# Performance work log

Measured on AMD Instinct MI355X. Metric: run time of the kernel, lower is better.

The kernel has to match this reference:

```python
import jax, jax.numpy as jnp
import numpy as np

ANGSTROM_TO_BOHR = 1.8897261258369282
CUTOFF = 5.2  # angstrom
N_SPECIES = 4  # H, C, N, O

# GFN1-xTB-style per-element constants for (H, C, N, O)
_ALPHA = np.array([2.209700, 1.247655, 1.524329, 1.845886], dtype=np.float32)
_Y_EFF = np.array([1.116244, 4.428763, 5.498808, 5.171786], dtype=np.float32)


def _smooth_cutoff(d, rc, eps=1e-10):
    # torchani 'smooth' cutoff: exp(1 - 1/(1 - (d/rc)^2)) for d < rc, else 0
    x2 = (d / rc) ** 2
    e = 1.0 - 1.0 / jnp.maximum(1.0 - x2, eps)
    return jnp.where(d < rc, jnp.exp(e), jnp.zeros_like(d))


def setup_inputs() -> dict:
    key = jax.random.key(0)
    k1, k2, k3 = jax.random.split(key, 3)
    M, A, P = 2048, 64, 8388608
    element_idxs = jax.random.randint(k1, (M, A), 0, N_SPECIES, dtype=jnp.int64)
    neighbor_idxs = jax.random.randint(k2, (2, P), 0, M * A, dtype=jnp.int64)
    distances = jax.random.uniform(k3, (P,), dtype=jnp.float32, minval=0.5, maxval=6.0)
    # precomputed pairwise parameter tables (buffers in the torch module)
    y_ab = jnp.asarray(np.outer(_Y_EFF, _Y_EFF))                 # [4,4]
    sqrt_alpha_ab = jnp.asarray(np.sqrt(np.outer(_ALPHA, _ALPHA)))  # [4,4]
    k_rep = np.full((N_SPECIES, N_SPECIES), 1.5, dtype=np.float32)
    k_rep[0, 0] = 1.0  # H-H
    k_rep_ab = jnp.asarray(k_rep)
    return {
        "element_idxs": element_idxs,
        "neighbor_idxs": neighbor_idxs,
        "distances": distances,
        "y_ab": y_ab,
        "sqrt_alpha_ab": sqrt_alpha_ab,
        "k_rep_ab": k_rep_ab,
    }


def reference(element_idxs, neighbor_idxs, distances, y_ab, sqrt_alpha_ab, k_rep_ab):
    M, A = element_idxs.shape
    d = jnp.clip(distances, 1e-7) * ANGSTROM_TO_BOHR  # [P] bohr
    species12 = element_idxs.reshape(-1)[neighbor_idxs]  # [2, P]
    s0, s1 = species12[0], species12[1]
    y = y_ab[s0, s1]                    # [P] gather
    sa = sqrt_alpha_ab[s0, s1]          # [P]
    kr = k_rep_ab[s0, s1]               # [P]
    rep = (y / d) * jnp.exp(-sa * d ** kr)
    rep = rep * _smooth_cutoff(d, CUTOFF * ANGSTROM_TO_BOHR)
    mol_idx = neighbor_idxs[0] // A     # [P]
    energies = jax.ops.segment_sum(rep, mol_idx, num_segments=M)  # [M]
    return energies
```

## Files before the change

kernel.cpp:

```cpp
#include <hip/hip_runtime.h>


#define AB_D 1.8897261258369282
#define L2E  1.4426950408889634f

__global__ __launch_bounds__(256) void pack_zero_kernel(
    const int* __restrict__ elem, int natoms, int nwords,
    unsigned* __restrict__ packed, float* __restrict__ out, int M)
{
    int g = blockIdx.x * blockDim.x + threadIdx.x;
    if (g < M) out[g] = 0.0f;
    if (packed != nullptr && g < nwords) {
        int base = g * 16;
        unsigned w = 0u;
        if (base + 16 <= natoms) {
            const int4* p = (const int4*)(elem + base);
            #pragma unroll
            for (int q = 0; q < 4; ++q) {
                int4 v = p[q];
                w |= ((unsigned)v.x & 3u) << (2 * (4 * q + 0));
                w |= ((unsigned)v.y & 3u) << (2 * (4 * q + 1));
                w |= ((unsigned)v.z & 3u) << (2 * (4 * q + 2));
                w |= ((unsigned)v.w & 3u) << (2 * (4 * q + 3));
            }
        } else {
            for (int j = 0; j < 16; ++j) {
                int a = base + j;
                unsigned s = (a < natoms) ? ((unsigned)elem[a] & 3u) : 0u;
                w |= s << (2 * j);
            }
        }
        packed[g] = w;
    }
}

__global__ __launch_bounds__(1024, 8) void rep_main_kernel(
    const int* __restrict__ nbr, const float* __restrict__ dist,
    const unsigned* __restrict__ packed_g,
    const float* __restrict__ y_ab, const float* __restrict__ sa_ab,
    const float* __restrict__ kr_ab,
    long long P, int M, int nwords, int ashift, int A,
    float* __restrict__ partials, float* __restrict__ out,
    int mode )
{
    extern __shared__ char smem[];
    float*  acc = (float*)smem;
    float2* tbl = (float2*)(smem + (size_t)M * 4);
    unsigned* pk = (unsigned*)(smem + (size_t)M * 4 + 16 * sizeof(float2));

    const int tid = threadIdx.x;
    const int nthr = blockDim.x;

    for (int m = tid; m < M; m += nthr) acc[m] = 0.0f;
    for (int w = tid; w < nwords; w += nthr) pk[w] = packed_g[w];
    if (tid < 16) {
        float sa = sa_ab[tid] * L2E;
        if (kr_ab[tid] == 1.0f) sa = -sa;
        tbl[tid] = make_float2(y_ab[tid], sa);
    }
    __syncthreads();

    const float ABf    = (float)AB_D;
    const float DMIN   = (float)(1e-7 * AB_D);
    const float RC     = (float)(5.2 * AB_D);
    const float RCINV  = (float)(1.0 / (5.2 * AB_D));
    const int* nb0 = nbr;
    const int* nb1 = nbr + P;

    auto process = [&](int a0, int a1, float draw) {
        float d = fmaxf(draw * ABf, DMIN);
        if (d < RC) {
            unsigned ua0 = (unsigned)a0, ua1 = (unsigned)a1;
            unsigned w0 = pk[ua0 >> 4];
            unsigned w1 = pk[ua1 >> 4];
            unsigned s0 = (w0 >> ((ua0 & 15u) * 2u)) & 3u;
            unsigned s1 = (w1 >> ((ua1 & 15u) * 2u)) & 3u;
            float2 t = tbl[s0 * 4u + s1];

            float sq   = __builtin_amdgcn_sqrtf(d);
            float fac  = (t.y < 0.0f) ? 1.0f : sq;
            float drep = d * fac;
            float x    = d * RCINV;
            float om   = fmaf(-x, x, 1.0f);
            float r    = __builtin_amdgcn_rcpf(om);
            float e    = fmaf(-L2E, r, L2E);
            float arg  = fmaf(-fabsf(t.y), drep, e);
            float ex   = __builtin_amdgcn_exp2f(arg);
            float rep  = t.x * __builtin_amdgcn_rcpf(d) * ex;

            unsigned mol = (ashift >= 0) ? (ua0 >> ashift) : (ua0 / (unsigned)A);
            atomicAdd(&acc[mol], rep);
        }
    };

    long long P4 = P >> 2;
    long long gstride = (long long)gridDim.x * nthr;
    for (long long q = (long long)blockIdx.x * nthr + tid; q < P4; q += gstride) {
        int4   i0 = ((const int4*)nb0)[q];
        int4   i1 = ((const int4*)nb1)[q];
        float4 dv = ((const float4*)dist)[q];
        process(i0.x, i1.x, dv.x);
        process(i0.y, i1.y, dv.y);
        process(i0.z, i1.z, dv.z);
        process(i0.w, i1.w, dv.w);
    }
    long long tail0 = P4 << 2;
    if (blockIdx.x == 0) {
        for (long long p = tail0 + tid; p < P; p += nthr)
            process(nb0[p], nb1[p], dist[p]);
    }
    __syncthreads();

    if (mode == 0) {
        float* row = partials + (size_t)blockIdx.x * (size_t)M;
        for (int m = tid; m < M; m += nthr) row[m] = acc[m];
    } else {
        for (int m = tid; m < M; m += nthr) {
            float v = acc[m];
            if (v != 0.0f) atomicAdd(&out[m], v);
        }
    }
}

__global__ __launch_bounds__(256) void reduce_kernel(
    const float* __restrict__ partials, float* __restrict__ out,
    int M, int nblk, int rows_per)
{
    int m = blockIdx.x * blockDim.x + threadIdx.x;
    if (m >= M) return;
    int r0 = blockIdx.y * rows_per;
    int r1 = r0 + rows_per;
    if (r1 > nblk) r1 = nblk;
    if (r0 >= r1) return;
    float s0 = 0.f, s1 = 0.f, s2 = 0.f, s3 = 0.f;
    int r = r0;
    for (; r + 3 < r1; r += 4) {
        s0 += partials[(size_t)(r + 0) * M + m];
        s1 += partials[(size_t)(r + 1) * M + m];
        s2 += partials[(size_t)(r + 2) * M + m];
        s3 += partials[(size_t)(r + 3) * M + m];
    }
    for (; r < r1; ++r) s0 += partials[(size_t)r * M + m];
    atomicAdd(&out[m], (s0 + s1) + (s2 + s3));
}

extern "C" void kernel_launch(void* const* d_in, const int* in_sizes, int n_in,
                              void* d_out, int out_size, void* d_ws, size_t ws_size,
                              hipStream_t stream)
{
    const int*   elem  = (const int*)d_in[0];
    const int*   nbr   = (const int*)d_in[1];
    const float* dist  = (const float*)d_in[2];
    const float* y_ab  = (const float*)d_in[3];
    const float* sa_ab = (const float*)d_in[4];
    const float* kr_ab = (const float*)d_in[5];
    float* out = (float*)d_out;

    const int natoms = in_sizes[0];
    const long long P = (long long)in_sizes[2];
    const int M = out_size;
    const int A = natoms / M;
    int ashift = -1;
    if (A > 0 && (A & (A - 1)) == 0) {
        int s = 0;
        while ((1 << s) < A) ++s;
        ashift = s;
    }
    const int nwords = (natoms + 15) / 16;

    size_t packed_bytes = ((size_t)nwords * 4 + 255) & ~(size_t)255;
    bool have_packed = (ws_size >= packed_bytes);
    unsigned* packed = have_packed ? (unsigned*)d_ws : nullptr;
    if (!have_packed) return;

    const int BLOCK = 1024;
    int nblk = 512;
    float* partials = nullptr;
    int mode = 1;
    {
        size_t avail = ws_size - packed_bytes;
        size_t rowb = (size_t)M * 4;
        long long maxrows = (long long)(avail / rowb);
        if (maxrows >= 64) {
            nblk = (int)(maxrows < 512 ? maxrows : 512);
            partials = (float*)((char*)d_ws + packed_bytes);
            mode = 0;
        }
    }

    {
        int total = (nwords > M) ? nwords : M;
        int g = (total + 255) / 256;
        hipLaunchKernelGGL(pack_zero_kernel, dim3(g), dim3(256), 0, stream,
                           elem, natoms, nwords, packed, out, M);
    }

    {
        size_t smem = (size_t)M * 4 + 16 * sizeof(float2) + (size_t)nwords * 4;
        hipLaunchKernelGGL(rep_main_kernel, dim3(nblk), dim3(BLOCK), smem, stream,
                           nbr, dist, packed, y_ab, sa_ab, kr_ab,
                           P, M, nwords, ashift, A, partials, out, mode);
    }

    if (mode == 0) {
        const int SPLIT = 32;
        int rows_per = (nblk + SPLIT - 1) / SPLIT;
        dim3 grid((M + 255) / 256, SPLIT);
        hipLaunchKernelGGL(reduce_kernel, grid, dim3(256), 0, stream,
                           partials, out, M, nblk, rows_per);
    }
}
```

Baseline: 154.7 us.

## Software-pipeline pair loads and make the per-pair cutoff math branchless

The grid-stride loop now prefetches the next iteration's index and distance vectors before processing the current ones, with a sched_barrier to keep the loads issued early. This is meant to hide global memory latency. The per-pair d<RC branch is removed: the cutoff factor is clamped via fmaxf(om,0), so out-of-range pairs give rcp(0)=inf, exp2(-inf)=0 and add zeros. That costs extra LDS atomics for pairs beyond the cutoff. Molecule index now uses a magic-multiply division instead of a shift or divide, which adds a 64-bit multiply per pair.

```diff
diff --git a/kernel.cpp b/kernel.cpp
--- a/kernel.cpp
+++ b/kernel.cpp
@@ -39,7 +39,7 @@
     const unsigned* __restrict__ packed_g,
     const float* __restrict__ y_ab, const float* __restrict__ sa_ab,
     const float* __restrict__ kr_ab,
-    long long P, int M, int nwords, int ashift, int A,
+    long long P, int M, int nwords, unsigned long long molMagic, int A,
     float* __restrict__ partials, float* __restrict__ out,
     int mode )
 {
@@ -60,54 +60,70 @@
     }
     __syncthreads();
 
-    const float ABf    = (float)AB_D;
-    const float DMIN   = (float)(1e-7 * AB_D);
-    const float RC     = (float)(5.2 * AB_D);
-    const float RCINV  = (float)(1.0 / (5.2 * AB_D));
-    const int* nb0 = nbr;
-    const int* nb1 = nbr + P;
-
-    auto process = [&](int a0, int a1, float draw) {
-        float d = fmaxf(draw * ABf, DMIN);
-        if (d < RC) {
-            unsigned ua0 = (unsigned)a0, ua1 = (unsigned)a1;
-            unsigned w0 = pk[ua0 >> 4];
-            unsigned w1 = pk[ua1 >> 4];
-            unsigned s0 = (w0 >> ((ua0 & 15u) * 2u)) & 3u;
-            unsigned s1 = (w1 >> ((ua1 & 15u) * 2u)) & 3u;
-            float2 t = tbl[s0 * 4u + s1];
-
-            float sq   = __builtin_amdgcn_sqrtf(d);
-            float fac  = (t.y < 0.0f) ? 1.0f : sq;
-            float drep = d * fac;
-            float x    = d * RCINV;
-            float om   = fmaf(-x, x, 1.0f);
-            float r    = __builtin_amdgcn_rcpf(om);
-            float e    = fmaf(-L2E, r, L2E);
-            float arg  = fmaf(-fabsf(t.y), drep, e);
-            float ex   = __builtin_amdgcn_exp2f(arg);
-            float rep  = t.x * __builtin_amdgcn_rcpf(d) * ex;
-
-            unsigned mol = (ashift >= 0) ? (ua0 >> ashift) : (ua0 / (unsigned)A);
-            atomicAdd(&acc[mol], rep);
-        }
+    const float ABf   = (float)AB_D;
+    const float DMIN  = (float)(1e-7 * AB_D);
+    const float RCINV = (float)(1.0 / (5.2 * AB_D));
+
+    const int4*   nb04 = (const int4*)nbr;
+    const int4*   nb14 = (const int4*)(nbr + P);
+    const float4* dv4  = (const float4*)dist;
+
+    auto pair = [&](unsigned ua0, unsigned ua1, float draw) {
+        unsigned w0 = pk[ua0 >> 4];
+        unsigned w1 = pk[ua1 >> 4];
+        unsigned s0 = (w0 >> ((ua0 & 15u) * 2u)) & 3u;
+        unsigned s1 = (w1 >> ((ua1 & 15u) * 2u)) & 3u;
+        float2 t = tbl[s0 * 4u + s1];
+        float d   = fmaxf(draw * ABf, DMIN);
+        float x   = d * RCINV;
+        float om  = fmaxf(fmaf(-x, x, 1.0f), 0.0f);
+        float r   = __builtin_amdgcn_rcpf(om);
+        float e   = fmaf(-L2E, r, L2E);
+        float sq  = __builtin_amdgcn_sqrtf(d);
+        float fac = (t.y < 0.0f) ? 1.0f : sq;
+        float arg = fmaf(-fabsf(t.y), d * fac, e);
+        float ex  = __builtin_amdgcn_exp2f(arg);
+        float rep = t.x * __builtin_amdgcn_rcpf(d) * ex;
+        unsigned mol = (unsigned)(((unsigned long long)ua0 * molMagic) >> 42);
+        atomicAdd(&acc[mol], rep);
+    };
+
+    auto process = [&](int4 i0, int4 i1, float4 dv) {
+        pair((unsigned)i0.x, (unsigned)i1.x, dv.x);
+        pair((unsigned)i0.y, (unsigned)i1.y, dv.y);
+        pair((unsigned)i0.z, (unsigned)i1.z, dv.z);
+        pair((unsigned)i0.w, (unsigned)i1.w, dv.w);
     };
 
     long long P4 = P >> 2;
     long long gstride = (long long)gridDim.x * nthr;
-    for (long long q = (long long)blockIdx.x * nthr + tid; q < P4; q += gstride) {
-        int4   i0 = ((const int4*)nb0)[q];
-        int4   i1 = ((const int4*)nb1)[q];
-        float4 dv = ((const float4*)dist)[q];
-        process(i0.x, i1.x, dv.x);
-        process(i0.y, i1.y, dv.y);
-        process(i0.z, i1.z, dv.z);
-        process(i0.w, i1.w, dv.w);
-    }
+    long long i = (long long)blockIdx.x * nthr + tid;
+
+    if (i < P4) {
+        int4   c0 = nb04[i];
+        int4   c1 = nb14[i];
+        float4 cd = dv4[i];
+        long long j = i + gstride;
+        while (true) {
+            bool more = (j < P4);
+            long long js = more ? j : i;
+            int4   n0 = nb04[js];
+            int4   n1 = nb14[js];
+            float4 nd = dv4[js];
+            __builtin_amdgcn_sched_barrier(0);
+            process(c0, c1, cd);
+            if (!more) break;
+            c0 = n0; c1 = n1; cd = nd;
+            j += gstride;
+        }
+    }
+
     long long tail0 = P4 << 2;
     if (blockIdx.x == 0) {
+        const int* nb0 = nbr;
+        const int* nb1 = nbr + P;
         for (long long p = tail0 + tid; p < P; p += nthr)
-            process(nb0[p], nb1[p], dist[p]);
+            pair((unsigned)nb0[p], (unsigned)nb1[p], dist[p]);
     }
     __syncthreads();
 
@@ -160,12 +176,10 @@
     const long long P = (long long)in_sizes[2];
     const int M = out_size;
     const int A = natoms / M;
-    int ashift = -1;
-    if (A > 0 && (A & (A - 1)) == 0) {
-        int s = 0;
-        while ((1 << s) < A) ++s;
-        ashift = s;
-    }
+    unsigned long long molMagic =
+        (A > 0) ? ((((unsigned long long)1 << 42) + (unsigned long long)A - 1)
+                   / (unsigned long long)A)
+                : 1ull;
     const int nwords = (natoms + 15) / 16;
 
     size_t packed_bytes = ((size_t)nwords * 4 + 255) & ~(size_t)255;
@@ -199,7 +213,7 @@
         size_t smem = (size_t)M * 4 + 16 * sizeof(float2) + (size_t)nwords * 4;
         hipLaunchKernelGGL(rep_main_kernel, dim3(nblk), dim3(BLOCK), smem, stream,
                            nbr, dist, packed, y_ab, sa_ab, kr_ab,
-                           P, M, nwords, ashift, A, partials, out, mode);
+                           P, M, nwords, molMagic, A, partials, out, mode);
     }
 
     if (mode == 0) {
```

After: 159.3 us. +3.0%, slower.
